# Performance work log

Hardware: AMD Instinct MI355X
Metric: run time of the kernel (lower is better)

## Reference

```python
import jax, jax.numpy as jnp
import numpy as np

B, V = 256, 128256


def setup_inputs() -> dict:
    key = jax.random.key(0)
    k1, k2, k3 = jax.random.split(key, 3)
    logits = jax.random.normal(k1, (B, V), dtype=jnp.float32)
    temperatures = jax.random.uniform(k2, (B,), dtype=jnp.float32, minval=0.1, maxval=1.5)
    # make a quarter of the batch greedy (temperature == 0) to exercise both paths
    temperatures = temperatures.at[::4].set(0.0)
    # uniform draws underlying the Exp(1) noise (torch: empty_like(probs).exponential_(1))
    u = jax.random.uniform(k3, (B, V), dtype=jnp.float32, minval=1e-30, maxval=1.0)
    return {"logits": logits, "temperatures": temperatures, "u": u}


def reference(logits, temperatures, u):
    logits = logits.astype(jnp.float32)
    greedy_mask = temperatures <= 1e-10                      # (B,)
    safe_t = jnp.where(greedy_mask, jnp.ones_like(temperatures), temperatures)
    scaled = logits / safe_t[:, None]                        # (B, V)
    probs = jax.nn.softmax(scaled, axis=-1)                  # (B, V)
    # Exp(1) noise from uniform draws; clamp matches torch's clamp_min_(1e-10)
    exp_noise = jnp.maximum(-jnp.log(u), 1e-10)              # (B, V)
    sample_tokens = jnp.argmax(probs / exp_noise, axis=-1)   # Gumbel-max style sampling
    greedy_tokens = jnp.argmax(logits, axis=-1)
    return jnp.where(greedy_mask, greedy_tokens, sample_tokens)
```

## Files before the change

### kernel.cpp

```cpp
#include <hip/hip_runtime.h>
#include <stdint.h>


#define T1 256
#define SEGF4 1024

__device__ __forceinline__ uint32_t order_f32(float f) {
    uint32_t u = __float_as_uint(f);
    return (u & 0x80000000u) ? ~u : (u | 0x80000000u);
}

__device__ __forceinline__ void upd(float s, int idx, float& best, int& bidx) {
    if (s > best || (s == best && idx < bidx)) { best = s; bidx = idx; }
}

__global__ __launch_bounds__(T1) void sampler_part_kernel(
        const float* __restrict__ logits,
        const float* __restrict__ temps,
        const float* __restrict__ u,
        unsigned long long* __restrict__ ws,
        int V, int B) {
    const int seg = blockIdx.x;
    const int row = blockIdx.y;
    const int nvec = V >> 2;
    const int lim = nvec - 1;
    const int tid = threadIdx.x;

    const int i0 = (seg * SEGF4) + tid;
    int ia = i0           > lim ? lim : i0;
    int ib = i0 + T1      > lim ? lim : i0 + T1;
    int ic = i0 + 2 * T1  > lim ? lim : i0 + 2 * T1;
    int id = i0 + 3 * T1  > lim ? lim : i0 + 3 * T1;

    const float t = temps[row];
    const bool greedy = (t <= 1e-10f);
    const float invT = greedy ? 1.0f : (1.4426950408889634f / t);
    const float CLMP = 1.4426950408889634e-10f;

    const size_t rowoff = (size_t)row * (size_t)V;
    const float4* lrow = reinterpret_cast<const float4*>(logits + rowoff);

    float best = -__builtin_inff();
    int bidx = 0x7fffffff;

    if (greedy) {
        float4 la = lrow[ia], lb = lrow[ib], lc = lrow[ic], ld = lrow[id];
        upd(la.x, 4*ia+0, best, bidx); upd(la.y, 4*ia+1, best, bidx);
        upd(la.z, 4*ia+2, best, bidx); upd(la.w, 4*ia+3, best, bidx);
        upd(lb.x, 4*ib+0, best, bidx); upd(lb.y, 4*ib+1, best, bidx);
        upd(lb.z, 4*ib+2, best, bidx); upd(lb.w, 4*ib+3, best, bidx);
        upd(lc.x, 4*ic+0, best, bidx); upd(lc.y, 4*ic+1, best, bidx);
        upd(lc.z, 4*ic+2, best, bidx); upd(lc.w, 4*ic+3, best, bidx);
        upd(ld.x, 4*id+0, best, bidx); upd(ld.y, 4*id+1, best, bidx);
        upd(ld.z, 4*id+2, best, bidx); upd(ld.w, 4*id+3, best, bidx);
    } else {
        const float4* urow = reinterpret_cast<const float4*>(u + rowoff);
        float4 la = lrow[ia], lb = lrow[ib], lc = lrow[ic], ld = lrow[id];
        float4 ua = urow[ia], ub = urow[ib], uc = urow[ic], ud = urow[id];
        float s;
        s = la.x * invT - __log2f(fmaxf(-__log2f(ua.x), CLMP)); upd(s, 4*ia+0, best, bidx);
        s = la.y * invT - __log2f(fmaxf(-__log2f(ua.y), CLMP)); upd(s, 4*ia+1, best, bidx);
        s = la.z * invT - __log2f(fmaxf(-__log2f(ua.z), CLMP)); upd(s, 4*ia+2, best, bidx);
        s = la.w * invT - __log2f(fmaxf(-__log2f(ua.w), CLMP)); upd(s, 4*ia+3, best, bidx);
        s = lb.x * invT - __log2f(fmaxf(-__log2f(ub.x), CLMP)); upd(s, 4*ib+0, best, bidx);
        s = lb.y * invT - __log2f(fmaxf(-__log2f(ub.y), CLMP)); upd(s, 4*ib+1, best, bidx);
        s = lb.z * invT - __log2f(fmaxf(-__log2f(ub.z), CLMP)); upd(s, 4*ib+2, best, bidx);
        s = lb.w * invT - __log2f(fmaxf(-__log2f(ub.w), CLMP)); upd(s, 4*ib+3, best, bidx);
        s = lc.x * invT - __log2f(fmaxf(-__log2f(uc.x), CLMP)); upd(s, 4*ic+0, best, bidx);
        s = lc.y * invT - __log2f(fmaxf(-__log2f(uc.y), CLMP)); upd(s, 4*ic+1, best, bidx);
        s = lc.z * invT - __log2f(fmaxf(-__log2f(uc.z), CLMP)); upd(s, 4*ic+2, best, bidx);
        s = lc.w * invT - __log2f(fmaxf(-__log2f(uc.w), CLMP)); upd(s, 4*ic+3, best, bidx);
        s = ld.x * invT - __log2f(fmaxf(-__log2f(ud.x), CLMP)); upd(s, 4*id+0, best, bidx);
        s = ld.y * invT - __log2f(fmaxf(-__log2f(ud.y), CLMP)); upd(s, 4*id+1, best, bidx);
        s = ld.z * invT - __log2f(fmaxf(-__log2f(ud.z), CLMP)); upd(s, 4*id+2, best, bidx);
        s = ld.w * invT - __log2f(fmaxf(-__log2f(ud.w), CLMP)); upd(s, 4*id+3, best, bidx);
    }

    unsigned long long key =
        ((unsigned long long)order_f32(best) << 32) | (unsigned long long)(~(uint32_t)bidx);

    #pragma unroll
    for (int off = 32; off > 0; off >>= 1) {
        unsigned long long other = __shfl_down(key, off, 64);
        if (other > key) key = other;
    }

    __shared__ unsigned long long smax;
    if (threadIdx.x == 0) smax = 0ull;
    __syncthreads();
    if ((threadIdx.x & 63) == 0) atomicMax(&smax, key);
    __syncthreads();
    if (threadIdx.x == 0) ws[(size_t)seg * B + row] = smax;
}

__global__ __launch_bounds__(256) void sampler_reduce_kernel(
        const unsigned long long* __restrict__ ws,
        int* __restrict__ out,
        int nseg, int B) {
    const int row = threadIdx.x;
    unsigned long long best = 0ull;
    #pragma unroll 8
    for (int s = 0; s < nseg; ++s) {
        unsigned long long k = ws[(size_t)s * B + row];
        if (k > best) best = k;
    }
    out[row] = (int)(~(uint32_t)(best & 0xffffffffull));
}

extern "C" void kernel_launch(void* const* d_in, const int* in_sizes, int n_in,
                              void* d_out, int out_size, void* d_ws, size_t ws_size,
                              hipStream_t stream) {
    const float* logits = (const float*)d_in[0];
    const float* temps  = (const float*)d_in[1];
    const float* u      = (const float*)d_in[2];
    int* out = (int*)d_out;
    unsigned long long* ws = (unsigned long long*)d_ws;

    const int B = in_sizes[1];
    const int V = in_sizes[0] / B;
    const int nvec = V >> 2;
    const int nseg = (nvec + SEGF4 - 1) / SEGF4;

    dim3 grid(nseg, B);
    sampler_part_kernel<<<grid, T1, 0, stream>>>(logits, temps, u, ws, V, B);
    sampler_reduce_kernel<<<1, B, 0, stream>>>(ws, out, nseg, B);
}
```

Baseline: 41.86 us.

## Fuse segment reduction into main kernel with last-block atomic counter

Replaces the two-kernel scheme (many small 1024-float4 segments per row, then a separate reduce kernel) with a single kernel. Each row is split into 8 large chunks that threads loop over. The last block to finish a row, found through an atomic counter, reduces the per-chunk keys and writes the result. This removes a kernel launch and shrinks the grid from about 32 to 8 blocks per row, which gives each block a longer streaming loop. The trade-offs are an extra memset launch for the counters, fence and atomic overhead, and fewer blocks overall (2048), which may limit memory-level parallelism.

```diff
diff --git a/kernel.cpp b/kernel.cpp
--- a/kernel.cpp
+++ b/kernel.cpp
@@ -2,8 +2,8 @@
 #include <stdint.h>
 
 
+#define SEGS 8
 #define T1 256
-#define SEGF4 1024
 
 __device__ __forceinline__ uint32_t order_f32(float f) {
     uint32_t u = __float_as_uint(f);
@@ -14,23 +14,21 @@
     if (s > best || (s == best && idx < bidx)) { best = s; bidx = idx; }
 }
 
-__global__ __launch_bounds__(T1) void sampler_part_kernel(
+__global__ __launch_bounds__(T1) void sampler_fused_kernel(
         const float* __restrict__ logits,
         const float* __restrict__ temps,
         const float* __restrict__ u,
-        unsigned long long* __restrict__ ws,
+        unsigned long long* __restrict__ keys,
+        unsigned int* __restrict__ cnt,
+        int* __restrict__ out,
         int V, int B) {
     const int seg = blockIdx.x;
     const int row = blockIdx.y;
     const int nvec = V >> 2;
-    const int lim = nvec - 1;
+    const int chunk = (nvec + SEGS - 1) / SEGS;
+    const int lo = seg * chunk;
+    const int hi = min(lo + chunk, nvec);
     const int tid = threadIdx.x;
-
-    const int i0 = (seg * SEGF4) + tid;
-    int ia = i0           > lim ? lim : i0;
-    int ib = i0 + T1      > lim ? lim : i0 + T1;
-    int ic = i0 + 2 * T1  > lim ? lim : i0 + 2 * T1;
-    int id = i0 + 3 * T1  > lim ? lim : i0 + 3 * T1;
 
     const float t = temps[row];
     const bool greedy = (t <= 1e-10f);
@@ -39,41 +37,49 @@
 
     const size_t rowoff = (size_t)row * (size_t)V;
     const float4* lrow = reinterpret_cast<const float4*>(logits + rowoff);
+    const float4* urow = reinterpret_cast<const float4*>(u + rowoff);
 
     float best = -__builtin_inff();
     int bidx = 0x7fffffff;
 
-    if (greedy) {
-        float4 la = lrow[ia], lb = lrow[ib], lc = lrow[ic], ld = lrow[id];
-        upd(la.x, 4*ia+0, best, bidx); upd(la.y, 4*ia+1, best, bidx);
-        upd(la.z, 4*ia+2, best, bidx); upd(la.w, 4*ia+3, best, bidx);
-        upd(lb.x, 4*ib+0, best, bidx); upd(lb.y, 4*ib+1, best, bidx);
-        upd(lb.z, 4*ib+2, best, bidx); upd(lb.w, 4*ib+3, best, bidx);
-        upd(lc.x, 4*ic+0, best, bidx); upd(lc.y, 4*ic+1, best, bidx);
-        upd(lc.z, 4*ic+2, best, bidx); upd(lc.w, 4*ic+3, best, bidx);
-        upd(ld.x, 4*id+0, best, bidx); upd(ld.y, 4*id+1, best, bidx);
-        upd(ld.z, 4*id+2, best, bidx); upd(ld.w, 4*id+3, best, bidx);
-    } else {
-        const float4* urow = reinterpret_cast<const float4*>(u + rowoff);
-        float4 la = lrow[ia], lb = lrow[ib], lc = lrow[ic], ld = lrow[id];
-        float4 ua = urow[ia], ub = urow[ib], uc = urow[ic], ud = urow[id];
-        float s;
-        s = la.x * invT - __log2f(fmaxf(-__log2f(ua.x), CLMP)); upd(s, 4*ia+0, best, bidx);
-        s = la.y * invT - __log2f(fmaxf(-__log2f(ua.y), CLMP)); upd(s, 4*ia+1, best, bidx);
-        s = la.z * invT - __log2f(fmaxf(-__log2f(ua.z), CLMP)); upd(s, 4*ia+2, best, bidx);
-        s = la.w * invT - __log2f(fmaxf(-__log2f(ua.w), CLMP)); upd(s, 4*ia+3, best, bidx);
-        s = lb.x * invT - __log2f(fmaxf(-__log2f(ub.x), CLMP)); upd(s, 4*ib+0, best, bidx);
-        s = lb.y * invT - __log2f(fmaxf(-__log2f(ub.y), CLMP)); upd(s, 4*ib+1, best, bidx);
-        s = lb.z * invT - __log2f(fmaxf(-__log2f(ub.z), CLMP)); upd(s, 4*ib+2, best, bidx);
-        s = lb.w * invT - __log2f(fmaxf(-__log2f(ub.w), CLMP)); upd(s, 4*ib+3, best, bidx);
-        s = lc.x * invT - __log2f(fmaxf(-__log2f(uc.x), CLMP)); upd(s, 4*ic+0, best, bidx);
-        s = lc.y * invT - __log2f(fmaxf(-__log2f(uc.y), CLMP)); upd(s, 4*ic+1, best, bidx);
-        s = lc.z * invT - __log2f(fmaxf(-__log2f(uc.z), CLMP)); upd(s, 4*ic+2, best, bidx);
-        s = lc.w * invT - __log2f(fmaxf(-__log2f(uc.w), CLMP)); upd(s, 4*ic+3, best, bidx);
-        s = ld.x * invT - __log2f(fmaxf(-__log2f(ud.x), CLMP)); upd(s, 4*id+0, best, bidx);
-        s = ld.y * invT - __log2f(fmaxf(-__log2f(ud.y), CLMP)); upd(s, 4*id+1, best, bidx);
-        s = ld.z * invT - __log2f(fmaxf(-__log2f(ud.z), CLMP)); upd(s, 4*id+2, best, bidx);
-        s = ld.w * invT - __log2f(fmaxf(-__log2f(ud.w), CLMP)); upd(s, 4*id+3, best, bidx);
+    for (int k = lo + tid; k < hi; k += 4 * T1) {
+        const int lim = hi - 1;
+        int ia = k;
+        int ib = k + T1     > lim ? lim : k + T1;
+        int ic = k + 2 * T1 > lim ? lim : k + 2 * T1;
+        int id = k + 3 * T1 > lim ? lim : k + 3 * T1;
+
+        if (greedy) {
+            float4 la = lrow[ia], lb = lrow[ib], lc = lrow[ic], ld = lrow[id];
+            upd(la.x, 4*ia+0, best, bidx); upd(la.y, 4*ia+1, best, bidx);
+            upd(la.z, 4*ia+2, best, bidx); upd(la.w, 4*ia+3, best, bidx);
+            upd(lb.x, 4*ib+0, best, bidx); upd(lb.y, 4*ib+1, best, bidx);
+            upd(lb.z, 4*ib+2, best, bidx); upd(lb.w, 4*ib+3, best, bidx);
+            upd(lc.x, 4*ic+0, best, bidx); upd(lc.y, 4*ic+1, best, bidx);
+            upd(lc.z, 4*ic+2, best, bidx); upd(lc.w, 4*ic+3, best, bidx);
+            upd(ld.x, 4*id+0, best, bidx); upd(ld.y, 4*id+1, best, bidx);
+            upd(ld.z, 4*id+2, best, bidx); upd(ld.w, 4*id+3, best, bidx);
+        } else {
+            float4 la = lrow[ia], lb = lrow[ib], lc = lrow[ic], ld = lrow[id];
+            float4 ua = urow[ia], ub = urow[ib], uc = urow[ic], ud = urow[id];
+            float s;
+            s = la.x * invT - __log2f(fmaxf(-__log2f(ua.x), CLMP)); upd(s, 4*ia+0, best, bidx);
+            s = la.y * invT - __log2f(fmaxf(-__log2f(ua.y), CLMP)); upd(s, 4*ia+1, best, bidx);
+            s = la.z * invT - __log2f(fmaxf(-__log2f(ua.z), CLMP)); upd(s, 4*ia+2, best, bidx);
+            s = la.w * invT - __log2f(fmaxf(-__log2f(ua.w), CLMP)); upd(s, 4*ia+3, best, bidx);
+            s = lb.x * invT - __log2f(fmaxf(-__log2f(ub.x), CLMP)); upd(s, 4*ib+0, best, bidx);
+            s = lb.y * invT - __log2f(fmaxf(-__log2f(ub.y), CLMP)); upd(s, 4*ib+1, best, bidx);
+            s = lb.z * invT - __log2f(fmaxf(-__log2f(ub.z), CLMP)); upd(s, 4*ib+2, best, bidx);
+            s = lb.w * invT - __log2f(fmaxf(-__log2f(ub.w), CLMP)); upd(s, 4*ib+3, best, bidx);
+            s = lc.x * invT - __log2f(fmaxf(-__log2f(uc.x), CLMP)); upd(s, 4*ic+0, best, bidx);
+            s = lc.y * invT - __log2f(fmaxf(-__log2f(uc.y), CLMP)); upd(s, 4*ic+1, best, bidx);
+            s = lc.z * invT - __log2f(fmaxf(-__log2f(uc.z), CLMP)); upd(s, 4*ic+2, best, bidx);
+            s = lc.w * invT - __log2f(fmaxf(-__log2f(uc.w), CLMP)); upd(s, 4*ic+3, best, bidx);
+            s = ld.x * invT - __log2f(fmaxf(-__log2f(ud.x), CLMP)); upd(s, 4*id+0, best, bidx);
+            s = ld.y * invT - __log2f(fmaxf(-__log2f(ud.y), CLMP)); upd(s, 4*id+1, best, bidx);
+            s = ld.z * invT - __log2f(fmaxf(-__log2f(ud.z), CLMP)); upd(s, 4*id+2, best, bidx);
+            s = ld.w * invT - __log2f(fmaxf(-__log2f(ud.w), CLMP)); upd(s, 4*id+3, best, bidx);
+        }
     }
 
     unsigned long long key =
@@ -86,25 +92,31 @@
     }
 
     __shared__ unsigned long long smax;
-    if (threadIdx.x == 0) smax = 0ull;
+    __shared__ unsigned int sold;
+    if (tid == 0) smax = 0ull;
     __syncthreads();
-    if ((threadIdx.x & 63) == 0) atomicMax(&smax, key);
+    if ((tid & 63) == 0) atomicMax(&smax, key);
     __syncthreads();
-    if (threadIdx.x == 0) ws[(size_t)seg * B + row] = smax;
-}
 
-__global__ __launch_bounds__(256) void sampler_reduce_kernel(
-        const unsigned long long* __restrict__ ws,
-        int* __restrict__ out,
-        int nseg, int B) {
-    const int row = threadIdx.x;
-    unsigned long long best = 0ull;
-    #pragma unroll 8
-    for (int s = 0; s < nseg; ++s) {
-        unsigned long long k = ws[(size_t)s * B + row];
-        if (k > best) best = k;
+    if (tid == 0) {
+        keys[(size_t)seg * B + row] = smax;
+        __threadfence();
+        sold = atomicAdd(&cnt[row], 1u);
     }
-    out[row] = (int)(~(uint32_t)(best & 0xffffffffull));
+    __syncthreads();
+
+    if (sold == SEGS - 1) {
+        if (tid == 0) {
+            __threadfence();
+            unsigned long long bestk = 0ull;
+            #pragma unroll
+            for (int s = 0; s < SEGS; ++s) {
+                unsigned long long k = atomicOr(&keys[(size_t)s * B + row], 0ull);
+                if (k > bestk) bestk = k;
+            }
+            out[row] = (int)(~(uint32_t)(bestk & 0xffffffffull));
+        }
+    }
 }
 
 extern "C" void kernel_launch(void* const* d_in, const int* in_sizes, int n_in,
@@ -114,14 +126,15 @@
     const float* temps  = (const float*)d_in[1];
     const float* u      = (const float*)d_in[2];
     int* out = (int*)d_out;
-    unsigned long long* ws = (unsigned long long*)d_ws;
 
     const int B = in_sizes[1];
     const int V = in_sizes[0] / B;
-    const int nvec = V >> 2;
-    const int nseg = (nvec + SEGF4 - 1) / SEGF4;
 
-    dim3 grid(nseg, B);
-    sampler_part_kernel<<<grid, T1, 0, stream>>>(logits, temps, u, ws, V, B);
-    sampler_reduce_kernel<<<1, B, 0, stream>>>(ws, out, nseg, B);
+    unsigned long long* keys = (unsigned long long*)d_ws;
+    unsigned int* cnt = (unsigned int*)((char*)d_ws + (size_t)SEGS * B * sizeof(unsigned long long));
+
+    hipMemsetAsync(cnt, 0, (size_t)B * sizeof(unsigned int), stream);
+
+    dim3 grid(SEGS, B);
+    sampler_fused_kernel<<<grid, T1, 0, stream>>>(logits, temps, u, keys, cnt, out, V, B);
 }
```

Result: slower. 135.1 us (+222.9%).
